# Kernel optimization log

Hardware: AMD Instinct MI355X
Metric: run time of the kernel (lower is better)

Reference implementation:

```python
import jax, jax.numpy as jnp
import numpy as np

DT_MIN, DT_MAX = 1e-3, 0.1
BSZ, SEQ, DM, DS = 8, 2048, 1024, 16


def setup_inputs() -> dict:
    key = jax.random.key(0)
    ks = jax.random.split(key, 8)
    x = jax.random.normal(ks[0], (BSZ, SEQ, DM), jnp.float32)
    a_log = jax.random.normal(ks[1], (DM, DS), jnp.float32) * -0.5
    b = jax.random.normal(ks[2], (DM, DS), jnp.float32) * 0.02
    c = jax.random.normal(ks[3], (DM, DS), jnp.float32) * 0.02
    dt_w = jax.random.normal(ks[4], (DM, DM), jnp.float32) * (1.0 / np.sqrt(DM))
    dt_b = jnp.zeros((DM,), jnp.float32)
    conv_w = jax.random.normal(ks[5], (DM, 1, 3), jnp.float32) * (1.0 / np.sqrt(3.0))
    conv_b = jnp.zeros((DM,), jnp.float32)
    return {"x": x, "a_log": a_log, "b": b, "c": c, "dt_w": dt_w, "dt_b": dt_b, "conv_w": conv_w, "conv_b": conv_b}


def _depthwise_conv(x, conv_w, conv_b):
    # x: (B,N,C) -> (B,C,N) depthwise conv k=3, pad=1 -> (B,N,C)
    xc = jnp.transpose(x, (0, 2, 1))
    y = jax.lax.conv_general_dilated(
        xc, conv_w, window_strides=(1,), padding=[(1, 1)],
        feature_group_count=xc.shape[1],
        dimension_numbers=("NCH", "OIH", "NCH"))
    y = y + conv_b[None, :, None]
    return jnp.transpose(y, (0, 2, 1))


def reference(x, a_log, b, c, dt_w, dt_b, conv_w, conv_b):
    Bn, N, C = x.shape
    D = a_log.shape[1]
    xf = _depthwise_conv(x, conv_w, conv_b)                      # (B,N,C)
    dt = jax.nn.sigmoid(xf @ dt_w.T + dt_b) * (DT_MAX - DT_MIN) + DT_MIN  # (B,N,C)
    A = -jax.nn.softplus(a_log)                                   # (C,D)

    def step(s, inp):
        xt, dtt = inp                                             # each (B,C)
        expA = jnp.exp(dtt[..., None] * A)                        # (B,C,D)
        s = expA * s + (dtt * xt)[..., None] * b                  # (B,C,D)
        y = jnp.einsum("bcd,cd->bc", s, c)
        return s, y

    s0 = jnp.zeros((Bn, C, D), x.dtype)
    xs = (jnp.transpose(xf, (1, 0, 2)), jnp.transpose(dt, (1, 0, 2)))
    _, ys = jax.lax.scan(step, s0, xs)                            # (N,B,C)
    return jnp.transpose(ys, (1, 0, 2))                           # (B,N,C)
```

## Files before the change

### kernel.cpp

```cpp
#include <hip/hip_runtime.h>
#include <stdint.h>

#define BSZ 8
#define SEQ 2048
#define DM 1024
#define DS 16
#define MROWS (BSZ * SEQ)
#define CHK 64
#define CLEN (SEQ / CHK)
#define LOG2E 1.4426950408889634f

typedef __bf16 bf16x8 __attribute__((ext_vector_type(8)));
typedef float f32x4 __attribute__((ext_vector_type(4)));

union F4 { float4 v; float f[4]; };

__device__ __forceinline__ uint16_t f2bf(float f) {
  uint32_t u = __float_as_uint(f);
  u += 0x7FFFu + ((u >> 16) & 1u);
  return (uint16_t)(u >> 16);
}

__device__ __forceinline__ uint32_t pack_h2(float a, float b) {
  _Float16 ha = (_Float16)a, hb = (_Float16)b;
  uint16_t ua = __builtin_bit_cast(uint16_t, ha);
  uint16_t ub = __builtin_bit_cast(uint16_t, hb);
  return (uint32_t)ua | ((uint32_t)ub << 16);
}
__device__ __forceinline__ float unpack_lo(uint32_t v) {
  return (float)__builtin_bit_cast(_Float16, (uint16_t)(v & 0xffffu));
}
__device__ __forceinline__ float unpack_hi(uint32_t v) {
  return (float)__builtin_bit_cast(_Float16, (uint16_t)(v >> 16));
}

__device__ __forceinline__ void async_cp16(const void* g, void* l) {
  __builtin_amdgcn_global_load_lds(
      (const __attribute__((address_space(1))) uint32_t*)(uintptr_t)g,
      (__attribute__((address_space(3))) uint32_t*)(uint32_t)(uintptr_t)l,
      16, 0, 0);
}

__global__ __launch_bounds__(256) void wprep_kernel(
    const float* __restrict__ w, uint16_t* __restrict__ wb) {
  int t = blockIdx.x * 256 + threadIdx.x;
  F4 u; u.v = *(const float4*)(w + (size_t)t * 4);
  uint32_t lo = f2bf(u.f[0]) | ((uint32_t)f2bf(u.f[1]) << 16);
  uint32_t hi = f2bf(u.f[2]) | ((uint32_t)f2bf(u.f[3]) << 16);
  *(uint2*)(wb + (size_t)t * 4) = make_uint2(lo, hi);
}

__global__ __launch_bounds__(256) void aprep_kernel(
    const float* __restrict__ a_log, const float* __restrict__ bm,
    const float* __restrict__ cm, float* __restrict__ A2c,
    float* __restrict__ A2t, float* __restrict__ cb2) {
  int e = blockIdx.x * 256 + threadIdx.x;
  float a = a_log[e];
  float A2 = -log1pf(__expf(a)) * LOG2E;
  A2c[e] = A2;
  cb2[e] = bm[e] * cm[e];
  int c = e >> 4, d = e & 15;
  int j = d >> 2, i = d & 3;
  A2t[((size_t)j * DM + c) * 4 + i] = A2;
}

__global__ __launch_bounds__(256) void conv_kernel(
    const float* __restrict__ x, const float* __restrict__ cw,
    const float* __restrict__ cb, uint16_t* __restrict__ xf) {
  int t = blockIdx.x * 256 + threadIdx.x;
  int cg = t & (DM / 4 - 1);
  int bn = t >> 8;
  int n = bn & (SEQ - 1);
  int c0 = cg * 4;
  const float* row = x + (size_t)bn * DM + c0;
  F4 xm, xc, xp;
  xm.v = make_float4(0.f, 0.f, 0.f, 0.f);
  xp.v = make_float4(0.f, 0.f, 0.f, 0.f);
  xc.v = *(const float4*)row;
  if (n > 0)       xm.v = *(const float4*)(row - DM);
  if (n < SEQ - 1) xp.v = *(const float4*)(row + DM);
  uint16_t o[4];
#pragma unroll
  for (int j = 0; j < 4; ++j) {
    int c = c0 + j;
    float v = cw[c * 3 + 0] * xm.f[j] + cw[c * 3 + 1] * xc.f[j] +
              cw[c * 3 + 2] * xp.f[j] + cb[c];
    o[j] = f2bf(v);
  }
  uint32_t lo = o[0] | ((uint32_t)o[1] << 16);
  uint32_t hi = o[2] | ((uint32_t)o[3] << 16);
  *(uint2*)(xf + (size_t)bn * DM + c0) = make_uint2(lo, hi);
}

__global__ __launch_bounds__(256) void gemm_kernel(
    const uint16_t* __restrict__ A,
    const uint16_t* __restrict__ B,
    const float* __restrict__ bias,
    uint32_t* __restrict__ ud) {
  __shared__ __align__(16) uint16_t As[128 * 64];
  __shared__ __align__(16) uint16_t Bs[128 * 64];
  const int tid = threadIdx.x;
  const int w = tid >> 6;
  const int L = tid & 63;
  const int wm = w & 1, wn = w >> 1;
  const int lane15 = L & 15, q = L >> 4;

  const int flat = blockIdx.y * gridDim.x + blockIdx.x;
  const int swz  = (flat & 7) * ((MROWS / 128 * DM / 128) / 8) + (flat >> 3);
  const int m0 = (swz >> 3) * 128;
  const int n0 = (swz & 7) * 128;

  const int lr = L >> 3;
  const int lc = (((L & 7) ^ lr)) * 8;
  const int r7 = lane15 & 7;

  f32x4 acc[4][4] = {};
  uint32_t xst[4][4][2];
  const int ktmatch = n0 + wn * 64;

  for (int kt = 0; kt < DM; kt += 64) {
#pragma unroll
    for (int r = 0; r < 4; ++r) {
      int R = (r * 4 + w) * 8;
      async_cp16(A + (size_t)(m0 + R + lr) * DM + kt + lc, &As[R * 64]);
    }
#pragma unroll
    for (int r = 0; r < 4; ++r) {
      int R = (r * 4 + w) * 8;
      async_cp16(B + (size_t)(n0 + R + lr) * DM + kt + lc, &Bs[R * 64]);
    }
    __syncthreads();

    if (kt == ktmatch) {
#pragma unroll
      for (int mi = 0; mi < 4; ++mi)
#pragma unroll
        for (int ni = 0; ni < 4; ++ni)
#pragma unroll
          for (int rp = 0; rp < 2; ++rp) {
            int row0 = wm * 64 + mi * 16 + q * 4 + rp * 2;
            int row1 = row0 + 1;
            int cc = ni * 16 + lane15;
            uint32_t e0 = As[row0 * 64 + (((cc >> 3) ^ (row0 & 7)) << 3) + (cc & 7)];
            uint32_t e1 = As[row1 * 64 + (((cc >> 3) ^ (row1 & 7)) << 3) + (cc & 7)];
            xst[mi][ni][rp] = e0 | (e1 << 16);
          }
    }

#pragma unroll
    for (int ks = 0; ks < 64; ks += 32) {
      bf16x8 af[4], bfr[4];
      const int jbase = ks >> 3;
#pragma unroll
      for (int mi = 0; mi < 4; ++mi)
        af[mi] = *(const bf16x8*)(As + (wm * 64 + mi * 16 + lane15) * 64 +
                                  (((jbase + q) ^ r7) << 3));
#pragma unroll
      for (int ni = 0; ni < 4; ++ni)
        bfr[ni] = *(const bf16x8*)(Bs + (wn * 64 + ni * 16 + lane15) * 64 +
                                   (((jbase + q) ^ r7) << 3));
#pragma unroll
      for (int mi = 0; mi < 4; ++mi)
#pragma unroll
        for (int ni = 0; ni < 4; ++ni)
          acc[mi][ni] = __builtin_amdgcn_mfma_f32_16x16x32_bf16(
              af[mi], bfr[ni], acc[mi][ni], 0, 0, 0);
    }
    __syncthreads();
  }

#pragma unroll
  for (int ni = 0; ni < 4; ++ni) {
    int col = n0 + wn * 64 + ni * 16 + lane15;
    float db = bias[col];
#pragma unroll
    for (int mi = 0; mi < 4; ++mi) {
      int rowb = m0 + wm * 64 + mi * 16 + q * 4;
#pragma unroll
      for (int r = 0; r < 4; ++r) {
        size_t idx = (size_t)(rowb + r) * DM + col;
        float z = acc[mi][ni][r] + db;
        float dtv = 0.099f / (1.f + __expf(-z)) + 0.001f;
        uint32_t p = xst[mi][ni][r >> 1];
        uint32_t bits = (r & 1) ? (p & 0xffff0000u) : (p << 16);
        float xfv = __uint_as_float(bits);
        ud[idx] = pack_h2(dtv * xfv, dtv);
      }
    }
  }
}


__global__ __launch_bounds__(256) void scan_part1(
    const uint32_t* __restrict__ ud, const float* __restrict__ A2c,
    float* __restrict__ F, float* __restrict__ Sdt) {
  const int c = blockIdx.x * 256 + threadIdx.x;
  const int k = blockIdx.y;
  const int b = blockIdx.z;
  const int n0 = k * CLEN;

  float A2[DS], s[DS];
#pragma unroll
  for (int j = 0; j < 4; ++j) {
    F4 ua; ua.v = *(const float4*)(A2c + (size_t)c * DS + j * 4);
#pragma unroll
    for (int i = 0; i < 4; ++i) {
      A2[j * 4 + i] = ua.f[i];
      s[j * 4 + i] = 0.f;
    }
  }

  const uint32_t* up = ud + ((size_t)b * SEQ + n0) * DM + c;
  uint32_t c0 = up[0];
  uint32_t c1 = up[DM];
  uint32_t c2 = up[2 * DM];
  float sdt = 0.f;

#pragma unroll 4
  for (int t = 0; t < CLEN; ++t) {
    int tn = (t + 3 < CLEN) ? t + 3 : CLEN - 1;
    uint32_t c3 = up[(size_t)tn * DM];
    float uv = unpack_lo(c0);
    float dtv = unpack_hi(c0);
    sdt += dtv;
#pragma unroll
    for (int d = 0; d < DS; ++d) {
      float e = __builtin_amdgcn_exp2f(dtv * A2[d]);
      s[d] = fmaf(e, s[d], uv);
    }
    c0 = c1; c1 = c2; c2 = c3;
  }

  const size_t kk = (size_t)b * CHK + k;
#pragma unroll
  for (int j = 0; j < 4; ++j) {
    F4 fo;
#pragma unroll
    for (int i = 0; i < 4; ++i) fo.f[i] = s[j * 4 + i];
    *(float4*)(F + ((kk * 4 + j) * DM + c) * 4) = fo.v;
  }
  Sdt[kk * DM + c] = sdt;
}

__global__ __launch_bounds__(256) void scan_combine(
    const float* __restrict__ F, float* __restrict__ Sin,
    const float* __restrict__ Sdt, const float* __restrict__ A2t) {
  const int t = blockIdx.x * 256 + threadIdx.x;
  const int b = blockIdx.y;
  const int c = (t >> 2) & (DM - 1);
  const float A2 = A2t[t];
  const size_t stride = (size_t)DM * DS;
  const size_t base = (size_t)b * CHK * stride + t;
  const size_t sbase = (size_t)b * CHK * DM + c;

  float fb[4], sb[4];
#pragma unroll
  for (int i = 0; i < 4; ++i) {
    int ki = (i < CHK) ? i : CHK - 1;
    fb[i] = F[base + (size_t)ki * stride];
    sb[i] = Sdt[sbase + (size_t)ki * DM];
  }

  float carry = 0.f;
#pragma unroll 4
  for (int k = 0; k < CHK; ++k) {
    int kn = (k + 4 < CHK) ? k + 4 : CHK - 1;
    float fnext = F[base + (size_t)kn * stride];
    float snext = Sdt[sbase + (size_t)kn * DM];
    float p = __builtin_amdgcn_exp2f(A2 * sb[0]);
    Sin[base + (size_t)k * stride] = carry;
    carry = fmaf(p, carry, fb[0]);
    fb[0] = fb[1]; fb[1] = fb[2]; fb[2] = fb[3]; fb[3] = fnext;
    sb[0] = sb[1]; sb[1] = sb[2]; sb[2] = sb[3]; sb[3] = snext;
  }
}

__global__ __launch_bounds__(256) void scan_part3(
    const uint32_t* __restrict__ ud, const float* __restrict__ A2c,
    const float* __restrict__ cb2m, const float* __restrict__ Sin,
    float* __restrict__ out) {
  const int c = blockIdx.x * 256 + threadIdx.x;
  const int k = blockIdx.y;
  const int b = blockIdx.z;
  const int n0 = k * CLEN;

  float A2[DS], cb2[DS], s[DS];
  const size_t kk = (size_t)b * CHK + k;
#pragma unroll
  for (int j = 0; j < 4; ++j) {
    F4 ua, uc, us;
    ua.v = *(const float4*)(A2c + (size_t)c * DS + j * 4);
    uc.v = *(const float4*)(cb2m + (size_t)c * DS + j * 4);
    us.v = *(const float4*)(Sin + ((kk * 4 + j) * DM + c) * 4);
#pragma unroll
    for (int i = 0; i < 4; ++i) {
      A2[j * 4 + i] = ua.f[i];
      cb2[j * 4 + i] = uc.f[i];
      s[j * 4 + i] = us.f[i];
    }
  }

  const uint32_t* up = ud + ((size_t)b * SEQ + n0) * DM + c;
  float* op = out + ((size_t)b * SEQ + n0) * DM + c;
  uint32_t c0 = up[0];
  uint32_t c1 = up[DM];
  uint32_t c2 = up[2 * DM];

#pragma unroll 4
  for (int t = 0; t < CLEN; ++t) {
    int tn = (t + 3 < CLEN) ? t + 3 : CLEN - 1;
    uint32_t c3 = up[(size_t)tn * DM];
    float uv = unpack_lo(c0);
    float dtv = unpack_hi(c0);
    float y0 = 0.f, y1 = 0.f;
#pragma unroll
    for (int d = 0; d < DS; d += 2) {
      float e0 = __builtin_amdgcn_exp2f(dtv * A2[d]);
      float e1 = __builtin_amdgcn_exp2f(dtv * A2[d + 1]);
      s[d] = fmaf(e0, s[d], uv);
      s[d + 1] = fmaf(e1, s[d + 1], uv);
      y0 = fmaf(cb2[d], s[d], y0);
      y1 = fmaf(cb2[d + 1], s[d + 1], y1);
    }
    op[(size_t)t * DM] = y0 + y1;
    c0 = c1; c1 = c2; c2 = c3;
  }
}

extern "C" void kernel_launch(void* const* d_in, const int* in_sizes, int n_in,
                              void* d_out, int out_size, void* d_ws, size_t ws_size,
                              hipStream_t stream) {
  const float* x     = (const float*)d_in[0];
  const float* a_log = (const float*)d_in[1];
  const float* bm    = (const float*)d_in[2];
  const float* cm    = (const float*)d_in[3];
  const float* dt_w  = (const float*)d_in[4];
  const float* dt_b  = (const float*)d_in[5];
  const float* cw    = (const float*)d_in[6];
  const float* cb    = (const float*)d_in[7];
  float* out = (float*)d_out;

  char* ws = (char*)d_ws;
  uint16_t* xf_bf = (uint16_t*)ws;
  uint16_t* w_bf  = (uint16_t*)(ws + (size_t)MROWS * DM * 2);
  float*    Sin   = (float*)ws;
  uint32_t* ud = (uint32_t*)(ws + (size_t)MROWS * DM * 2 + (size_t)DM * DM * 2);
  float* Fbuf = (float*)(ud + (size_t)MROWS * DM);
  float* Sdt  = Fbuf + (size_t)BSZ * CHK * DM * DS;
  float* A2c  = Sdt + (size_t)BSZ * CHK * DM;
  float* A2t  = A2c + (size_t)DM * DS;
  float* cb2  = A2t + (size_t)DM * DS;

  hipLaunchKernelGGL(wprep_kernel, dim3(DM * DM / 1024), dim3(256), 0, stream,
                     dt_w, w_bf);
  hipLaunchKernelGGL(aprep_kernel, dim3(DM * DS / 256), dim3(256), 0, stream,
                     a_log, bm, cm, A2c, A2t, cb2);
  hipLaunchKernelGGL(conv_kernel, dim3(MROWS * DM / 1024), dim3(256), 0, stream,
                     x, cw, cb, xf_bf);
  hipLaunchKernelGGL(gemm_kernel, dim3(DM / 128, MROWS / 128), dim3(256), 0,
                     stream, xf_bf, w_bf, dt_b, ud);
  hipLaunchKernelGGL(scan_part1, dim3(DM / 256, CHK, BSZ), dim3(256), 0, stream,
                     ud, A2c, Fbuf, Sdt);
  hipLaunchKernelGGL(scan_combine, dim3(DM * DS / 256, BSZ), dim3(256), 0,
                     stream, Fbuf, Sin, Sdt, A2t);
  hipLaunchKernelGGL(scan_part3, dim3(DM / 256, CHK, BSZ), dim3(256), 0, stream,
                     ud, A2c, cb2, Sin, out);
}
```

Before: 276.4 us.

## Double-buffer 256x256 GEMM tiles with async prefetch and halve scan chunk count

Enlarges the dt GEMM tile to 256x256 with 512 threads and double-buffered shared memory, prefetching the next-but-one K slice while computing. Global loads and MFMA work overlap through manual vmcnt waits and barriers, and MFMA issue priority is raised during compute. The scan chunk count also drops from 64 to 32, which means fewer, longer chunks. The cost is more shared memory and registers per block and a smaller grid, and the new chunk count changes the parallelism and combine cost of the scan.

```diff
diff --git a/kernel.cpp b/kernel.cpp
--- a/kernel.cpp
+++ b/kernel.cpp
@@ -6,9 +6,13 @@
 #define DM 1024
 #define DS 16
 #define MROWS (BSZ * SEQ)
-#define CHK 64
+#define CHK 32
 #define CLEN (SEQ / CHK)
 #define LOG2E 1.4426950408889634f
+
+#define BM 256
+#define BN 256
+#define BK 64
 
 typedef __bf16 bf16x8 __attribute__((ext_vector_type(8)));
 typedef float f32x4 __attribute__((ext_vector_type(4)));
@@ -92,13 +96,13 @@
   *(uint2*)(xf + (size_t)bn * DM + c0) = make_uint2(lo, hi);
 }
 
-__global__ __launch_bounds__(256) void gemm_kernel(
+__global__ __launch_bounds__(512) void gemm_kernel(
     const uint16_t* __restrict__ A,
     const uint16_t* __restrict__ B,
     const float* __restrict__ bias,
     uint32_t* __restrict__ ud) {
-  __shared__ __align__(16) uint16_t As[128 * 64];
-  __shared__ __align__(16) uint16_t Bs[128 * 64];
+  __shared__ __align__(16) uint16_t As[2][BM * BK];
+  __shared__ __align__(16) uint16_t Bs[2][BN * BK];
   const int tid = threadIdx.x;
   const int w = tid >> 6;
   const int L = tid & 63;
@@ -106,67 +110,91 @@
   const int lane15 = L & 15, q = L >> 4;
 
   const int flat = blockIdx.y * gridDim.x + blockIdx.x;
-  const int swz  = (flat & 7) * ((MROWS / 128 * DM / 128) / 8) + (flat >> 3);
-  const int m0 = (swz >> 3) * 128;
-  const int n0 = (swz & 7) * 128;
+  const int swz = (flat & 7) * 32 + (flat >> 3);
+  const int m0 = (swz >> 2) * BM;
+  const int n0 = (swz & 3) * BN;
 
   const int lr = L >> 3;
-  const int lc = (((L & 7) ^ lr)) * 8;
+  const int lc = ((L & 7) ^ lr) * 8;
   const int r7 = lane15 & 7;
 
-  f32x4 acc[4][4] = {};
-  uint32_t xst[4][4][2];
-  const int ktmatch = n0 + wn * 64;
-
-  for (int kt = 0; kt < DM; kt += 64) {
+  f32x4 acc[8][4] = {};
+  uint32_t xst[8][4][2];
+  const int tstar = (n0 + wn * 64) >> 6;
+
+  auto stage = [&](int kt, int p) {
 #pragma unroll
     for (int r = 0; r < 4; ++r) {
-      int R = (r * 4 + w) * 8;
-      async_cp16(A + (size_t)(m0 + R + lr) * DM + kt + lc, &As[R * 64]);
+      int R = (r * 8 + w) * 8;
+      async_cp16(A + (size_t)(m0 + R + lr) * DM + kt + lc, &As[p][R * 64]);
     }
 #pragma unroll
     for (int r = 0; r < 4; ++r) {
-      int R = (r * 4 + w) * 8;
-      async_cp16(B + (size_t)(n0 + R + lr) * DM + kt + lc, &Bs[R * 64]);
-    }
-    __syncthreads();
-
-    if (kt == ktmatch) {
-#pragma unroll
-      for (int mi = 0; mi < 4; ++mi)
+      int R = (r * 8 + w) * 8;
+      async_cp16(B + (size_t)(n0 + R + lr) * DM + kt + lc, &Bs[p][R * 64]);
+    }
+  };
+
+  stage(0, 0);
+  stage(BK, 1);
+
+  for (int t = 0; t < DM / BK; ++t) {
+    const int p = t & 1;
+    if (t < DM / BK - 1)
+      asm volatile("s_waitcnt vmcnt(8)\ns_barrier" ::: "memory");
+    else
+      asm volatile("s_waitcnt vmcnt(0)\ns_barrier" ::: "memory");
+
+    if (t == tstar) {
+#pragma unroll
+      for (int mi = 0; mi < 8; ++mi)
 #pragma unroll
         for (int ni = 0; ni < 4; ++ni)
 #pragma unroll
           for (int rp = 0; rp < 2; ++rp) {
-            int row0 = wm * 64 + mi * 16 + q * 4 + rp * 2;
+            int row0 = wm * 128 + mi * 16 + q * 4 + rp * 2;
             int row1 = row0 + 1;
             int cc = ni * 16 + lane15;
-            uint32_t e0 = As[row0 * 64 + (((cc >> 3) ^ (row0 & 7)) << 3) + (cc & 7)];
-            uint32_t e1 = As[row1 * 64 + (((cc >> 3) ^ (row1 & 7)) << 3) + (cc & 7)];
+            uint32_t e0 =
+                As[p][row0 * 64 + (((cc >> 3) ^ (row0 & 7)) << 3) + (cc & 7)];
+            uint32_t e1 =
+                As[p][row1 * 64 + (((cc >> 3) ^ (row1 & 7)) << 3) + (cc & 7)];
             xst[mi][ni][rp] = e0 | (e1 << 16);
           }
     }
 
-#pragma unroll
-    for (int ks = 0; ks < 64; ks += 32) {
-      bf16x8 af[4], bfr[4];
-      const int jbase = ks >> 3;
-#pragma unroll
-      for (int mi = 0; mi < 4; ++mi)
-        af[mi] = *(const bf16x8*)(As + (wm * 64 + mi * 16 + lane15) * 64 +
-                                  (((jbase + q) ^ r7) << 3));
-#pragma unroll
-      for (int ni = 0; ni < 4; ++ni)
-        bfr[ni] = *(const bf16x8*)(Bs + (wn * 64 + ni * 16 + lane15) * 64 +
-                                   (((jbase + q) ^ r7) << 3));
-#pragma unroll
-      for (int mi = 0; mi < 4; ++mi)
+    bf16x8 bfr[4][2];
+#pragma unroll
+    for (int ni = 0; ni < 4; ++ni)
+#pragma unroll
+      for (int ks = 0; ks < 2; ++ks)
+        bfr[ni][ks] = *(const bf16x8*)(&Bs[p][(wn * 64 + ni * 16 + lane15) * 64 +
+                                              ((((ks << 2) + q) ^ r7) << 3)]);
+
+#pragma unroll
+    for (int f = 0; f < 4; ++f) {
+      bf16x8 af[2][2];
+#pragma unroll
+      for (int u2 = 0; u2 < 2; ++u2)
+#pragma unroll
+        for (int ks = 0; ks < 2; ++ks)
+          af[u2][ks] = *(const bf16x8*)(&As[p][(wm * 128 + (f * 2 + u2) * 16 +
+                                                lane15) * 64 +
+                                               ((((ks << 2) + q) ^ r7) << 3)]);
+      __builtin_amdgcn_s_setprio(1);
+#pragma unroll
+      for (int u2 = 0; u2 < 2; ++u2)
 #pragma unroll
         for (int ni = 0; ni < 4; ++ni)
-          acc[mi][ni] = __builtin_amdgcn_mfma_f32_16x16x32_bf16(
-              af[mi], bfr[ni], acc[mi][ni], 0, 0, 0);
-    }
-    __syncthreads();
+#pragma unroll
+          for (int ks = 0; ks < 2; ++ks)
+            acc[f * 2 + u2][ni] = __builtin_amdgcn_mfma_f32_16x16x32_bf16(
+                af[u2][ks], bfr[ni][ks], acc[f * 2 + u2][ni], 0, 0, 0);
+      __builtin_amdgcn_s_setprio(0);
+    }
+
+    asm volatile("s_barrier" ::: "memory");
+    if (t < DM / BK - 2) stage((t + 2) * BK, p);
   }
 
 #pragma unroll
@@ -174,15 +202,15 @@
     int col = n0 + wn * 64 + ni * 16 + lane15;
     float db = bias[col];
 #pragma unroll
-    for (int mi = 0; mi < 4; ++mi) {
-      int rowb = m0 + wm * 64 + mi * 16 + q * 4;
+    for (int mi = 0; mi < 8; ++mi) {
+      int rowb = m0 + wm * 128 + mi * 16 + q * 4;
 #pragma unroll
       for (int r = 0; r < 4; ++r) {
         size_t idx = (size_t)(rowb + r) * DM + col;
         float z = acc[mi][ni][r] + db;
         float dtv = 0.099f / (1.f + __expf(-z)) + 0.001f;
-        uint32_t p = xst[mi][ni][r >> 1];
-        uint32_t bits = (r & 1) ? (p & 0xffff0000u) : (p << 16);
+        uint32_t pk = xst[mi][ni][r >> 1];
+        uint32_t bits = (r & 1) ? (pk & 0xffff0000u) : (pk << 16);
         float xfv = __uint_as_float(bits);
         ud[idx] = pack_h2(dtv * xfv, dtv);
       }
@@ -357,7 +385,7 @@
                      a_log, bm, cm, A2c, A2t, cb2);
   hipLaunchKernelGGL(conv_kernel, dim3(MROWS * DM / 1024), dim3(256), 0, stream,
                      x, cw, cb, xf_bf);
-  hipLaunchKernelGGL(gemm_kernel, dim3(DM / 128, MROWS / 128), dim3(256), 0,
+  hipLaunchKernelGGL(gemm_kernel, dim3(DM / BN, MROWS / BM), dim3(512), 0,
                      stream, xf_bf, w_bf, dt_b, ud);
   hipLaunchKernelGGL(scan_part1, dim3(DM / 256, CHK, BSZ), dim3(256), 0, stream,
                      ud, A2c, Fbuf, Sdt);
```

New measurement: 376.1 us. 36.1% more time.
